# Performance work log

Hardware: AMD Instinct MI355X
Metric: run time of the kernel (lower is better)

## Reference

```python
import jax, jax.numpy as jnp
import numpy as np
from jax import lax

K = 3  # kernel_size

def _conv1d(inp, w, b, padding):
    # inp: [B, Cin, W], w: [Cout, Cin, K]
    y = lax.conv_general_dilated(inp, w, (1,), padding,
                                 dimension_numbers=('NCH', 'OIH', 'NCH'))
    return y + b[None, :, None]


def setup_inputs() -> dict:
    key = jax.random.key(0)
    ks = jax.random.split(key, 10)
    B, C, H, W = 8, 3, 512, 2048
    s = 0.1
    return {
        'x':  jax.random.normal(ks[0], (B, C, H, W), dtype=jnp.float32),
        'w1': jax.random.normal(ks[1], (5, 3, K),  dtype=jnp.float32) * s,
        'b1': jax.random.normal(ks[2], (5,),       dtype=jnp.float32) * s,
        'w2': jax.random.normal(ks[3], (10, 5, K), dtype=jnp.float32) * s,
        'b2': jax.random.normal(ks[4], (10,),      dtype=jnp.float32) * s,
        'wl': jax.random.normal(ks[5], (10, 12, K), dtype=jnp.float32) * s,
        'bl': jax.random.normal(ks[6], (10,),       dtype=jnp.float32) * s,
        'wo': jax.random.normal(ks[7], (1, 10),    dtype=jnp.float32) * s,  # 1x1 conv2d weight
        'bo': jax.random.normal(ks[8], (1,),       dtype=jnp.float32) * s,
    }


def reference(x, w1, b1, w2, b2, wl, bl, wo, bo):
    # x: [B, 3, num_steps, W]
    # Step 0: conv_first on stack([x[:,0,-1], x[:,1,0], x[:,2,0]])
    first_in = jnp.stack([x[:, 0, -1, :], x[:, 1, 0, :], x[:, 2, 0, :]], axis=1)  # [B,3,W]
    h = jax.nn.relu(_conv1d(first_in, w1, b1, 'VALID'))          # [B,5,W-2]
    h = jax.nn.relu(_conv1d(h, w2, b2, [(1, 1)]))                # [B,10,W-2] ('same')
    row0 = jnp.pad(h, ((0, 0), (0, 0), (1, 1)))                  # write into [:,:,0,1:-1]

    # Recurrence over steps 1..num_steps-1 (strict data dependence -> lax.scan)
    def step(prev, xi):
        # prev: [B,10,W], xi: [B,2,W]
        inp = jnp.concatenate([prev, xi], axis=1)                # [B,12,W]
        y = jax.nn.relu(_conv1d(inp, wl, bl, 'VALID'))           # [B,10,W-2]
        row = jnp.pad(y, ((0, 0), (0, 0), (1, 1)))               # [B,10,W]
        return row, row

    xs = jnp.moveaxis(x[:, 1:3, 1:, :], 2, 0)                    # [num_steps-1, B, 2, W]
    _, rows = lax.scan(step, row0, xs)                           # [num_steps-1, B, 10, W]

    pred = jnp.concatenate([row0[None], rows], axis=0)           # [num_steps, B, 10, W]
    pred = jnp.moveaxis(pred, 0, 2)                              # [B, 10, num_steps, W]

    # conv_to_result: 1x1 Conv2d, 10 -> 1 channels
    out = jnp.einsum('bchw,oc->bohw', pred, wo) + bo[None, :, None, None]
    return out
```

## Files before the change

kernel.cpp:

```cpp
#include <hip/hip_runtime.h>
#include <cstdint>

#define W 2048
#define H 512
#define ABASE 0
#define BBASE (2050*4)
#define BUFD  (2050*4 + 2052*4)
#define NWAVE 16

typedef __fp16 h2    __attribute__((ext_vector_type(2)));
typedef __fp16 f16x8 __attribute__((ext_vector_type(8)));
typedef float  f32x16 __attribute__((ext_vector_type(16)));

static __device__ __forceinline__ h2 as_h2(uint32_t u){ union{uint32_t u; h2 h;} x; x.u=u; return x.h; }
static __device__ __forceinline__ uint32_t as_u32(h2 h){ union{uint32_t u; h2 h;} x; x.h=h; return x.u; }

__global__ __launch_bounds__(1024, 1) void recurrent_kernel(
    const float* __restrict__ x,
    const float* __restrict__ w1, const float* __restrict__ b1,
    const float* __restrict__ w2, const float* __restrict__ b2,
    const float* __restrict__ wl, const float* __restrict__ bl,
    const float* __restrict__ wo, const float* __restrict__ bo,
    float* __restrict__ out)
{
    extern __shared__ uint32_t lds[];
    const int tid  = threadIdx.x;
    const int b    = blockIdx.x;
    const int lane = tid & 63;
    const int wv   = tid >> 6;
    const int m    = lane & 31;
    const int hh   = lane >> 5;

    for (int i = tid; i < 2*BUFD + NWAVE; i += 1024) lds[i] = 0;

    f16x8 afrag[3];
    #pragma unroll
    for (int tap = 0; tap < 3; ++tap)
        #pragma unroll
        for (int j = 0; j < 8; ++j) {
            int k = 8*hh + j;
            float v = (m < 10 && k < 12) ? wl[(m*12 + k)*3 + tap] : 0.f;
            afrag[tap][j] = (__fp16)v;
        }
    h2 wop0, wop1, wop2;
    if (hh == 0) {
        wop0 = __builtin_amdgcn_cvt_pkrtz(wo[0], wo[1]);
        wop1 = __builtin_amdgcn_cvt_pkrtz(wo[2], wo[3]);
        wop2 = __builtin_amdgcn_cvt_pkrtz(wo[8], wo[9]);
    } else {
        wop0 = __builtin_amdgcn_cvt_pkrtz(wo[4], wo[5]);
        wop1 = __builtin_amdgcn_cvt_pkrtz(wo[6], wo[7]);
        wop2 = __builtin_amdgcn_cvt_pkrtz(0.f, 0.f);
    }
    f32x16 bias16;
    #pragma unroll
    for (int r = 0; r < 16; ++r) {
        int ch = (r & 3) + 8*(r >> 2) + 4*hh;
        bias16[r] = (r < 8 && ch < 10) ? bl[ch] : 0.f;
    }
    const float bov = bo[0];
    const int bpaddr = (lane ^ 32) << 2;
    const h2 hz = {(__fp16)0.f, (__fp16)0.f};

    const float* x1b = x + (((size_t)b*3 + 1)*H)*W;
    const float* x2b = x + (((size_t)b*3 + 2)*H)*W;
    float* outb = out + (size_t)b*H*W;

    const int base_n = wv*128 + m;
    const int rdi = (hh ? BBASE : ABASE) + 4*base_n;
    uint32_t* fl = lds + 2*BUFD;
    const int na = (wv == 0)       ? wv : wv - 1;
    const int nb = (wv == NWAVE-1) ? wv : wv + 1;

    __syncthreads();

    {
        const float* f0p = x + (((size_t)b*3 + 0)*H + (H-1))*W;
        const float* f1p = x1b;
        const float* f2p = x2b;
        float fi[3][6];
        const int v0 = 2*tid - 1;
        #pragma unroll
        for (int l = 0; l < 6; ++l) {
            int v = v0 + l;
            bool ok = (v >= 0) && (v < W);
            fi[0][l] = ok ? f0p[v] : 0.f;
            fi[1][l] = ok ? f1p[v] : 0.f;
            fi[2][l] = ok ? f2p[v] : 0.f;
        }
        float h1v[5][4];
        #pragma unroll
        for (int c = 0; c < 5; ++c)
            #pragma unroll
            for (int i6 = 0; i6 < 4; ++i6) {
                int u = v0 + i6;
                float a = b1[c];
                #pragma unroll
                for (int j = 0; j < 3; ++j)
                    #pragma unroll
                    for (int k = 0; k < 3; ++k)
                        a += w1[(c*3 + j)*3 + k] * fi[j][i6 + k];
                h1v[c][i6] = (u >= 0 && u <= W-3) ? fmaxf(a, 0.f) : 0.f;
            }
        #pragma unroll
        for (int mm = 0; mm < 2; ++mm) {
            int w = 2*tid + 1 + mm;
            if (w <= W - 2) {
                float h2c[10];
                #pragma unroll
                for (int c2 = 0; c2 < 10; ++c2) {
                    float a = b2[c2];
                    #pragma unroll
                    for (int c = 0; c < 5; ++c)
                        #pragma unroll
                        for (int k = 0; k < 3; ++k)
                            a += w2[(c2*5 + c)*3 + k] * h1v[c][mm + k];
                    h2c[c2] = fmaxf(a, 0.f);
                }
                uint32_t* ra = lds + ABASE + 4*(w + 1);
                uint4 wr;
                wr.x = as_u32(__builtin_amdgcn_cvt_pkrtz(h2c[0], h2c[1]));
                wr.y = as_u32(__builtin_amdgcn_cvt_pkrtz(h2c[2], h2c[3]));
                wr.z = as_u32(__builtin_amdgcn_cvt_pkrtz(h2c[4], h2c[5]));
                wr.w = as_u32(__builtin_amdgcn_cvt_pkrtz(h2c[6], h2c[7]));
                *(uint4*)ra = wr;
                lds[BBASE + 4*(w + 1)] = as_u32(__builtin_amdgcn_cvt_pkrtz(h2c[8], h2c[9]));
            }
        }
        #pragma unroll
        for (int i = 0; i < 2; ++i) {
            int p = tid + 1024*i;
            lds[BBASE + 4*(p + 1) + 1] = as_u32(__builtin_amdgcn_cvt_pkrtz(x1b[W + p], x2b[W + p]));
        }
    }
    __syncthreads();

    {
        h2 wo01 = __builtin_amdgcn_cvt_pkrtz(wo[0], wo[1]);
        h2 wo23 = __builtin_amdgcn_cvt_pkrtz(wo[2], wo[3]);
        h2 wo45 = __builtin_amdgcn_cvt_pkrtz(wo[4], wo[5]);
        h2 wo67 = __builtin_amdgcn_cvt_pkrtz(wo[6], wo[7]);
        h2 wo89 = __builtin_amdgcn_cvt_pkrtz(wo[8], wo[9]);
        #pragma unroll
        for (int i = 0; i < 2; ++i) {
            int p = 2*tid + i;
            const uint32_t* ra = lds + ABASE + 4*(p + 1);
            uint4 a = *(const uint4*)ra;
            uint32_t e = lds[BBASE + 4*(p + 1)];
            float s = __builtin_amdgcn_fdot2(wo01, as_h2(a.x), bov, false);
            s = __builtin_amdgcn_fdot2(wo23, as_h2(a.y), s, false);
            s = __builtin_amdgcn_fdot2(wo45, as_h2(a.z), s, false);
            s = __builtin_amdgcn_fdot2(wo67, as_h2(a.w), s, false);
            s = __builtin_amdgcn_fdot2(wo89, as_h2(e),   s, false);
            outb[p] = s;
        }
    }

    #pragma unroll 1
    for (int t = 1; t < H; ++t) {
        const uint32_t* rb = lds + ((t - 1) & 1)*BUFD;
        uint32_t*       wb = lds + (t & 1)*BUFD;

        float xf1[2], xf2[2];
        const bool pf = (t + 1 < H);
        if (pf) {
            const float* r1 = x1b + (size_t)(t + 1)*W + 128*wv + lane;
            const float* r2 = x2b + (size_t)(t + 1)*W + 128*wv + lane;
            xf1[0] = r1[0];  xf1[1] = r1[64];
            xf2[0] = r2[0];  xf2[1] = r2[64];
        }

        if (t >= 2) {
            const uint32_t need = (uint32_t)(t - 1);
            while (__hip_atomic_load(&fl[na], __ATOMIC_ACQUIRE, __HIP_MEMORY_SCOPE_WORKGROUP) < need ||
                   __hip_atomic_load(&fl[nb], __ATOMIC_ACQUIRE, __HIP_MEMORY_SCOPE_WORKGROUP) < need)
                __builtin_amdgcn_s_sleep(1);
        }

        uint4 bu[4][3];
        #pragma unroll
        for (int ti = 0; ti < 4; ++ti)
            #pragma unroll
            for (int tap = 0; tap < 3; ++tap)
                bu[ti][tap] = *(const uint4*)(rb + rdi + 128*ti + 4*tap);

        uint32_t stash[4][3];
        float pv[4];
        #pragma unroll
        for (int ti = 0; ti < 4; ++ti) {
            union { uint4 u; f16x8 v; } c0, c1, c2;
            c0.u = bu[ti][0]; c1.u = bu[ti][1]; c2.u = bu[ti][2];
            f32x16 acc = __builtin_amdgcn_mfma_f32_32x32x16_f16(afrag[0], c0.v, bias16, 0, 0, 0);
            acc = __builtin_amdgcn_mfma_f32_32x32x16_f16(afrag[1], c1.v, acc, 0, 0, 0);
            acc = __builtin_amdgcn_mfma_f32_32x32x16_f16(afrag[2], c2.v, acc, 0, 0, 0);
            h2 p0 = __builtin_elementwise_max(__builtin_amdgcn_cvt_pkrtz(acc[0], acc[1]), hz);
            h2 p1 = __builtin_elementwise_max(__builtin_amdgcn_cvt_pkrtz(acc[2], acc[3]), hz);
            h2 p2 = __builtin_elementwise_max(__builtin_amdgcn_cvt_pkrtz(acc[4], acc[5]), hz);
            stash[ti][0] = as_u32(p0); stash[ti][1] = as_u32(p1); stash[ti][2] = as_u32(p2);
            float pc = __builtin_amdgcn_fdot2(wop2, p2,
                       __builtin_amdgcn_fdot2(wop1, p1,
                       __builtin_amdgcn_fdot2(wop0, p0, 0.f, false), false), false);
            int pi = __builtin_amdgcn_ds_bpermute(bpaddr, __builtin_bit_cast(int, pc));
            pv[ti] = pc + __builtin_bit_cast(float, pi);
        }

        #pragma unroll
        for (int ti = 0; ti < 4; ++ti) {
            const int n = base_n + 32*ti;
            if (n != 0 && n != W-1) {
                uint32_t* rp = wb + ABASE + 4*(n + 1) + 2*hh;
                uint2 wr; wr.x = stash[ti][0]; wr.y = stash[ti][1];
                *(uint2*)rp = wr;
                if (hh == 0) wb[BBASE + 4*(n + 1)] = stash[ti][2];
            }
        }
        if (pf) {
            const int p0 = 128*wv + lane;
            wb[BBASE + 4*(p0 + 1) + 1]      = as_u32(__builtin_amdgcn_cvt_pkrtz(xf1[0], xf2[0]));
            wb[BBASE + 4*(p0 + 64 + 1) + 1] = as_u32(__builtin_amdgcn_cvt_pkrtz(xf1[1], xf2[1]));
        }

        if (lane == 0)
            __hip_atomic_store(&fl[wv], (uint32_t)t, __ATOMIC_RELEASE, __HIP_MEMORY_SCOPE_WORKGROUP);

        #pragma unroll
        for (int i = 0; i < 2; ++i) {
            const int ti = 2*hh + i;
            const int n = base_n + 32*ti;
            float val = (n == 0 || n == W-1) ? bov : pv[ti] + bov;
            outb[(size_t)t*W + n] = val;
        }
    }
}

extern "C" void kernel_launch(void* const* d_in, const int* in_sizes, int n_in,
                              void* d_out, int out_size, void* d_ws, size_t ws_size,
                              hipStream_t stream)
{
    const float* x  = (const float*)d_in[0];
    const float* w1 = (const float*)d_in[1];
    const float* b1 = (const float*)d_in[2];
    const float* w2 = (const float*)d_in[3];
    const float* b2 = (const float*)d_in[4];
    const float* wl = (const float*)d_in[5];
    const float* bl = (const float*)d_in[6];
    const float* wo = (const float*)d_in[7];
    const float* bo = (const float*)d_in[8];
    float* out = (float*)d_out;

    const int shbytes = (2 * BUFD + NWAVE) * sizeof(uint32_t);
    hipFuncSetAttribute((const void*)recurrent_kernel,
                        hipFuncAttributeMaxDynamicSharedMemorySize, shbytes);
    recurrent_kernel<<<8, 1024, shbytes, stream>>>(x, w1, b1, w2, b2, wl, bl, wo, bo, out);
}
```

Before: 893.7 us.

## Split each batch row across two workgroups with global-memory halo exchange

Each batch's width is now split into two halves, each handled by its own 512-thread workgroup, so 16 workgroups run instead of 8. At every step the boundary columns are swapped between the paired workgroups through a workspace buffer, using agent-scope atomics and spin waits. The goal is to use more compute units and shorten the per-step critical path inside each workgroup. In exchange, each step adds a cross-CU global-memory handshake on the recurrence's critical path, and the kernel now depends on both blocks of a pair being resident at the same time.

```diff
diff --git a/kernel.cpp b/kernel.cpp
--- a/kernel.cpp
+++ b/kernel.cpp
@@ -3,10 +3,13 @@
 
 #define W 2048
 #define H 512
+#define NPOS 1024
+#define NW 8
+#define NSLOT 1026
 #define ABASE 0
-#define BBASE (2050*4)
-#define BUFD  (2050*4 + 2052*4)
-#define NWAVE 16
+#define BBASE (NSLOT*4)
+#define BUFD  10248
+#define FLOFF (2*BUFD)
 
 typedef __fp16 h2    __attribute__((ext_vector_type(2)));
 typedef __fp16 f16x8 __attribute__((ext_vector_type(8)));
@@ -15,23 +18,25 @@
 static __device__ __forceinline__ h2 as_h2(uint32_t u){ union{uint32_t u; h2 h;} x; x.u=u; return x.h; }
 static __device__ __forceinline__ uint32_t as_u32(h2 h){ union{uint32_t u; h2 h;} x; x.h=h; return x.u; }
 
-__global__ __launch_bounds__(1024, 1) void recurrent_kernel(
+__global__ __launch_bounds__(512, 1) void recurrent_kernel(
     const float* __restrict__ x,
     const float* __restrict__ w1, const float* __restrict__ b1,
     const float* __restrict__ w2, const float* __restrict__ b2,
     const float* __restrict__ wl, const float* __restrict__ bl,
     const float* __restrict__ wo, const float* __restrict__ bo,
-    float* __restrict__ out)
+    float* __restrict__ out, uint32_t* __restrict__ ws)
 {
     extern __shared__ uint32_t lds[];
     const int tid  = threadIdx.x;
-    const int b    = blockIdx.x;
+    const int b    = blockIdx.x & 7;
+    const int h    = blockIdx.x >> 3;
+    const int start= h * NPOS;
     const int lane = tid & 63;
-    const int wv   = tid >> 6;
+    const int wvL  = tid >> 6;
     const int m    = lane & 31;
     const int hh   = lane >> 5;
 
-    for (int i = tid; i < 2*BUFD + NWAVE; i += 1024) lds[i] = 0;
+    for (int i = tid; i < 2*BUFD + NW; i += 512) lds[i] = 0;
 
     f16x8 afrag[3];
     #pragma unroll
@@ -66,108 +71,97 @@
     const float* x2b = x + (((size_t)b*3 + 2)*H)*W;
     float* outb = out + (size_t)b*H*W;
 
-    const int base_n = wv*128 + m;
+    const int base_n = wvL*128 + m;
     const int rdi = (hh ? BBASE : ABASE) + 4*base_n;
-    uint32_t* fl = lds + 2*BUFD;
-    const int na = (wv == 0)       ? wv : wv - 1;
-    const int nb = (wv == NWAVE-1) ? wv : wv + 1;
+    const int wA_ = ABASE + 4*(base_n + 1) + 2*hh;
+    const int wB_ = BBASE + 4*(base_n + 1);
+    const int xw_ = BBASE + 4*(128*wvL + lane + 1) + 1;
+    uint32_t* fl = lds + FLOFF;
+    const int na = (wvL == 0)    ? wvL : wvL - 1;
+    const int nb = (wvL == NW-1) ? wvL : wvL + 1;
+
+    const bool has_rem  = (h == 0) ? (wvL == NW-1) : (wvL == 0);
+    const int  gslot    = (h == 0) ? (NSLOT-1) : 0;
+    const int  gcol     = (h == 0) ? NPOS : (NPOS-1);
+    const int  prodlane = (h == 0) ? 31 : 0;
+    uint32_t* rec_m = ws + (b*2 + h)*64;
+    uint32_t* rec_o = ws + (b*2 + (1-h))*64;
 
     __syncthreads();
 
-    {
-        const float* f0p = x + (((size_t)b*3 + 0)*H + (H-1))*W;
-        const float* f1p = x1b;
-        const float* f2p = x2b;
-        float fi[3][6];
-        const int v0 = 2*tid - 1;
-        #pragma unroll
-        for (int l = 0; l < 6; ++l) {
-            int v = v0 + l;
+    for (int idx = tid; idx < NSLOT; idx += 512) {
+        const int p = start + idx - 1;
+        float fi[3][5];
+        #pragma unroll
+        for (int l = 0; l < 5; ++l) {
+            int v = p - 2 + l;
             bool ok = (v >= 0) && (v < W);
-            fi[0][l] = ok ? f0p[v] : 0.f;
-            fi[1][l] = ok ? f1p[v] : 0.f;
-            fi[2][l] = ok ? f2p[v] : 0.f;
-        }
-        float h1v[5][4];
+            fi[0][l] = ok ? x[(((size_t)b*3 + 0)*H + (H-1))*W + v] : 0.f;
+            fi[1][l] = ok ? x1b[v] : 0.f;
+            fi[2][l] = ok ? x2b[v] : 0.f;
+        }
+        float h1v[5][3];
         #pragma unroll
         for (int c = 0; c < 5; ++c)
             #pragma unroll
-            for (int i6 = 0; i6 < 4; ++i6) {
-                int u = v0 + i6;
+            for (int i3 = 0; i3 < 3; ++i3) {
+                int u = p - 2 + i3;
                 float a = b1[c];
                 #pragma unroll
                 for (int j = 0; j < 3; ++j)
                     #pragma unroll
                     for (int k = 0; k < 3; ++k)
-                        a += w1[(c*3 + j)*3 + k] * fi[j][i6 + k];
-                h1v[c][i6] = (u >= 0 && u <= W-3) ? fmaxf(a, 0.f) : 0.f;
-            }
-        #pragma unroll
-        for (int mm = 0; mm < 2; ++mm) {
-            int w = 2*tid + 1 + mm;
-            if (w <= W - 2) {
-                float h2c[10];
+                        a += w1[(c*3 + j)*3 + k] * fi[j][i3 + k];
+                h1v[c][i3] = (u >= 0 && u <= W-3) ? fmaxf(a, 0.f) : 0.f;
+            }
+        const bool valid = (p >= 1) && (p <= W-2);
+        float h2c[10];
+        #pragma unroll
+        for (int c2 = 0; c2 < 10; ++c2) {
+            float a = b2[c2];
+            #pragma unroll
+            for (int c = 0; c < 5; ++c)
                 #pragma unroll
-                for (int c2 = 0; c2 < 10; ++c2) {
-                    float a = b2[c2];
-                    #pragma unroll
-                    for (int c = 0; c < 5; ++c)
-                        #pragma unroll
-                        for (int k = 0; k < 3; ++k)
-                            a += w2[(c2*5 + c)*3 + k] * h1v[c][mm + k];
-                    h2c[c2] = fmaxf(a, 0.f);
-                }
-                uint32_t* ra = lds + ABASE + 4*(w + 1);
-                uint4 wr;
-                wr.x = as_u32(__builtin_amdgcn_cvt_pkrtz(h2c[0], h2c[1]));
-                wr.y = as_u32(__builtin_amdgcn_cvt_pkrtz(h2c[2], h2c[3]));
-                wr.z = as_u32(__builtin_amdgcn_cvt_pkrtz(h2c[4], h2c[5]));
-                wr.w = as_u32(__builtin_amdgcn_cvt_pkrtz(h2c[6], h2c[7]));
-                *(uint4*)ra = wr;
-                lds[BBASE + 4*(w + 1)] = as_u32(__builtin_amdgcn_cvt_pkrtz(h2c[8], h2c[9]));
-            }
-        }
-        #pragma unroll
-        for (int i = 0; i < 2; ++i) {
-            int p = tid + 1024*i;
-            lds[BBASE + 4*(p + 1) + 1] = as_u32(__builtin_amdgcn_cvt_pkrtz(x1b[W + p], x2b[W + p]));
+                for (int k = 0; k < 3; ++k)
+                    a += w2[(c2*5 + c)*3 + k] * h1v[c][k];
+            h2c[c2] = valid ? fmaxf(a, 0.f) : 0.f;
+        }
+        uint4 wr;
+        wr.x = as_u32(__builtin_amdgcn_cvt_pkrtz(h2c[0], h2c[1]));
+        wr.y = as_u32(__builtin_amdgcn_cvt_pkrtz(h2c[2], h2c[3]));
+        wr.z = as_u32(__builtin_amdgcn_cvt_pkrtz(h2c[4], h2c[5]));
+        wr.w = as_u32(__builtin_amdgcn_cvt_pkrtz(h2c[6], h2c[7]));
+        *(uint4*)(lds + ABASE + 4*idx) = wr;
+        lds[BBASE + 4*idx] = as_u32(__builtin_amdgcn_cvt_pkrtz(h2c[8], h2c[9]));
+        bool okp = (p >= 0) && (p < W);
+        lds[BBASE + 4*idx + 1] = okp
+            ? as_u32(__builtin_amdgcn_cvt_pkrtz(x1b[W + p], x2b[W + p])) : 0u;
+        if (idx >= 1 && idx <= NPOS) {
+            float s = bov;
+            #pragma unroll
+            for (int c = 0; c < 10; ++c) s += wo[c]*h2c[c];
+            outb[p] = s;
         }
     }
     __syncthreads();
-
-    {
-        h2 wo01 = __builtin_amdgcn_cvt_pkrtz(wo[0], wo[1]);
-        h2 wo23 = __builtin_amdgcn_cvt_pkrtz(wo[2], wo[3]);
-        h2 wo45 = __builtin_amdgcn_cvt_pkrtz(wo[4], wo[5]);
-        h2 wo67 = __builtin_amdgcn_cvt_pkrtz(wo[6], wo[7]);
-        h2 wo89 = __builtin_amdgcn_cvt_pkrtz(wo[8], wo[9]);
-        #pragma unroll
-        for (int i = 0; i < 2; ++i) {
-            int p = 2*tid + i;
-            const uint32_t* ra = lds + ABASE + 4*(p + 1);
-            uint4 a = *(const uint4*)ra;
-            uint32_t e = lds[BBASE + 4*(p + 1)];
-            float s = __builtin_amdgcn_fdot2(wo01, as_h2(a.x), bov, false);
-            s = __builtin_amdgcn_fdot2(wo23, as_h2(a.y), s, false);
-            s = __builtin_amdgcn_fdot2(wo45, as_h2(a.z), s, false);
-            s = __builtin_amdgcn_fdot2(wo67, as_h2(a.w), s, false);
-            s = __builtin_amdgcn_fdot2(wo89, as_h2(e),   s, false);
-            outb[p] = s;
-        }
-    }
 
     #pragma unroll 1
     for (int t = 1; t < H; ++t) {
         const uint32_t* rb = lds + ((t - 1) & 1)*BUFD;
         uint32_t*       wb = lds + (t & 1)*BUFD;
 
-        float xf1[2], xf2[2];
+        float xf1[2], xf2[2], xg1 = 0.f, xg2 = 0.f;
         const bool pf = (t + 1 < H);
         if (pf) {
-            const float* r1 = x1b + (size_t)(t + 1)*W + 128*wv + lane;
-            const float* r2 = x2b + (size_t)(t + 1)*W + 128*wv + lane;
+            const float* r1 = x1b + (size_t)(t + 1)*W + start + 128*wvL + lane;
+            const float* r2 = x2b + (size_t)(t + 1)*W + start + 128*wvL + lane;
             xf1[0] = r1[0];  xf1[1] = r1[64];
             xf2[0] = r2[0];  xf2[1] = r2[64];
+            if (has_rem && lane == 0) {
+                xg1 = x1b[(size_t)(t + 1)*W + start + gcol - (h ? -1 : 0)*0 + (h ? -1025 : 0)*0 + ((h==0)?NPOS:-1)];
+                xg1 = x1b[(size_t)(t + 1)*W + (start + ((h==0)?NPOS:-1))];
+                xg2 = x2b[(size_t)(t + 1)*W + (start + ((h==0)?NPOS:-1))];
+            }
         }
 
         if (t >= 2) {
@@ -175,6 +169,24 @@
             while (__hip_atomic_load(&fl[na], __ATOMIC_ACQUIRE, __HIP_MEMORY_SCOPE_WORKGROUP) < need ||
                    __hip_atomic_load(&fl[nb], __ATOMIC_ACQUIRE, __HIP_MEMORY_SCOPE_WORKGROUP) < need)
                 __builtin_amdgcn_s_sleep(1);
+        }
+        if (has_rem && t >= 2) {
+            const int pr = (t - 1) & 1;
+            uint64_t* q2p = (uint64_t*)(rec_o + 12 + 8*pr);
+            uint64_t q2;
+            while ((uint32_t)((q2 = __hip_atomic_load(q2p, __ATOMIC_ACQUIRE, __HIP_MEMORY_SCOPE_AGENT)) >> 32)
+                   < (uint32_t)(t - 1))
+                __builtin_amdgcn_s_sleep(2);
+            if (lane == 0) {
+                uint64_t q0 = __hip_atomic_load((uint64_t*)(rec_o +  8 + 8*pr), __ATOMIC_RELAXED, __HIP_MEMORY_SCOPE_AGENT);
+                uint64_t q1 = __hip_atomic_load((uint64_t*)(rec_o + 10 + 8*pr), __ATOMIC_RELAXED, __HIP_MEMORY_SCOPE_AGENT);
+                uint32_t* rbw = const_cast<uint32_t*>(rb);
+                uint4 g;
+                g.x = (uint32_t)q0; g.y = (uint32_t)(q0 >> 32);
+                g.z = (uint32_t)q1; g.w = (uint32_t)(q1 >> 32);
+                *(uint4*)(rbw + ABASE + 4*gslot) = g;
+                rbw[BBASE + 4*gslot] = (uint32_t)q2;
+            }
         }
 
         uint4 bu[4][3];
@@ -204,31 +216,49 @@
             pv[ti] = pc + __builtin_bit_cast(float, pi);
         }
 
+        if (has_rem) {
+            uint32_t s0e = h ? stash[0][0] : stash[3][0];
+            uint32_t s1e = h ? stash[0][1] : stash[3][1];
+            uint32_t s2e = h ? stash[0][2] : stash[3][2];
+            uint32_t o0 = (uint32_t)__builtin_amdgcn_ds_bpermute(bpaddr, (int)s0e);
+            uint32_t o1 = (uint32_t)__builtin_amdgcn_ds_bpermute(bpaddr, (int)s1e);
+            if (lane == prodlane) {
+                const int pw = t & 1;
+                uint64_t q0 = (uint64_t)s0e | ((uint64_t)s1e << 32);
+                uint64_t q1 = (uint64_t)o0  | ((uint64_t)o1  << 32);
+                uint64_t q2 = (uint64_t)s2e | ((uint64_t)(uint32_t)t << 32);
+                __hip_atomic_store((uint64_t*)(rec_m +  8 + 8*pw), q0, __ATOMIC_RELAXED, __HIP_MEMORY_SCOPE_AGENT);
+                __hip_atomic_store((uint64_t*)(rec_m + 10 + 8*pw), q1, __ATOMIC_RELAXED, __HIP_MEMORY_SCOPE_AGENT);
+                __hip_atomic_store((uint64_t*)(rec_m + 12 + 8*pw), q2, __ATOMIC_RELEASE, __HIP_MEMORY_SCOPE_AGENT);
+            }
+        }
+
         #pragma unroll
         for (int ti = 0; ti < 4; ++ti) {
-            const int n = base_n + 32*ti;
-            if (n != 0 && n != W-1) {
-                uint32_t* rp = wb + ABASE + 4*(n + 1) + 2*hh;
+            const int ng = start + base_n + 32*ti;
+            if (ng != 0 && ng != W-1) {
+                uint32_t* rp = wb + wA_ + 128*ti;
                 uint2 wr; wr.x = stash[ti][0]; wr.y = stash[ti][1];
                 *(uint2*)rp = wr;
-                if (hh == 0) wb[BBASE + 4*(n + 1)] = stash[ti][2];
+                if (hh == 0) wb[wB_ + 128*ti] = stash[ti][2];
             }
         }
         if (pf) {
-            const int p0 = 128*wv + lane;
-            wb[BBASE + 4*(p0 + 1) + 1]      = as_u32(__builtin_amdgcn_cvt_pkrtz(xf1[0], xf2[0]));
-            wb[BBASE + 4*(p0 + 64 + 1) + 1] = as_u32(__builtin_amdgcn_cvt_pkrtz(xf1[1], xf2[1]));
+            wb[xw_]       = as_u32(__builtin_amdgcn_cvt_pkrtz(xf1[0], xf2[0]));
+            wb[xw_ + 256] = as_u32(__builtin_amdgcn_cvt_pkrtz(xf1[1], xf2[1]));
+            if (has_rem && lane == 0)
+                wb[BBASE + 4*gslot + 1] = as_u32(__builtin_amdgcn_cvt_pkrtz(xg1, xg2));
         }
 
         if (lane == 0)
-            __hip_atomic_store(&fl[wv], (uint32_t)t, __ATOMIC_RELEASE, __HIP_MEMORY_SCOPE_WORKGROUP);
+            __hip_atomic_store(&fl[wvL], (uint32_t)t, __ATOMIC_RELEASE, __HIP_MEMORY_SCOPE_WORKGROUP);
 
         #pragma unroll
         for (int i = 0; i < 2; ++i) {
             const int ti = 2*hh + i;
-            const int n = base_n + 32*ti;
-            float val = (n == 0 || n == W-1) ? bov : pv[ti] + bov;
-            outb[(size_t)t*W + n] = val;
+            const int ng = start + base_n + 32*ti;
+            float val = (ng == 0 || ng == W-1) ? bov : pv[ti] + bov;
+            outb[(size_t)t*W + ng] = val;
         }
     }
 }
@@ -248,8 +278,11 @@
     const float* bo = (const float*)d_in[8];
     float* out = (float*)d_out;
 
-    const int shbytes = (2 * BUFD + NWAVE) * sizeof(uint32_t);
+    hipMemsetAsync(d_ws, 0, 4096, stream);
+
+    const int shbytes = (2*BUFD + NW) * sizeof(uint32_t);
     hipFuncSetAttribute((const void*)recurrent_kernel,
                         hipFuncAttributeMaxDynamicSharedMemorySize, shbytes);
-    recurrent_kernel<<<8, 1024, shbytes, stream>>>(x, w1, b1, w2, b2, wl, bl, wo, bo, out);
+    recurrent_kernel<<<16, 512, shbytes, stream>>>(x, w1, b1, w2, b2, wl, bl, wo, bo,
+                                                   out, (uint32_t*)d_ws);
 }
```

After: 1.421 ms. +59.0%, slower.
